# Optimization experiments

Hardware: AMD Instinct MI355X
Metric: run time of the kernel (lower is better)

The kernel has to match this reference:

```python
import jax, jax.numpy as jnp
import numpy as np

TEMP = 0.5
EPS = 1e-12


def setup_inputs() -> dict:
    key = jax.random.key(0)
    k1, k2, k3 = jax.random.split(key, 3)
    B, D = 2048, 512
    f_seq = jax.random.normal(k1, (B, 4, D), dtype=jnp.float32)
    f_spa = jax.random.normal(k2, (B, 4, D), dtype=jnp.float32)
    W = jax.random.normal(k3, (2 * D, D), dtype=jnp.float32) * 0.02
    b = jnp.zeros((D,), dtype=jnp.float32)
    return {"f_seq": f_seq, "f_spa": f_spa, "W": W, "b": b}


def _project_all(f, W, b):
    # pairs: (0,2), (1,2), (3,2) -> concat along batch dim => [3B, D]
    B = f.shape[0]
    left = jnp.transpose(f[:, jnp.array([0, 1, 3]), :], (1, 0, 2)).reshape(3 * B, -1)
    right = jnp.broadcast_to(f[:, 2, :][None], (3, B, f.shape[-1])).reshape(3 * B, -1)
    return jnp.concatenate([left, right], axis=-1) @ W + b


def reference(f_seq, f_spa, W, b):
    B = f_seq.shape[0]
    v_spa = _project_all(f_spa, W, b)  # [3B, D]
    v_seq = _project_all(f_seq, W, b)  # [3B, D]

    def normalize(x):
        n = jnp.sqrt(jnp.sum(x * x, axis=1, keepdims=True))
        return x / jnp.maximum(n, EPS)

    z = jnp.concatenate([normalize(v_spa), normalize(v_seq)], axis=0)  # [6B, D]
    sim = z @ z.T  # cosine sim of unit vectors, [6B, 6B]
    half = 3 * B
    idx = jnp.arange(half)
    pos = jnp.concatenate([sim[idx, idx + half], sim[idx + half, idx]])  # [6B]
    e = jnp.exp(sim / TEMP)
    denom = jnp.sum(e, axis=1) - jnp.diagonal(e)  # neg_mask zeros the diagonal
    loss = jnp.sum(-(pos / TEMP) + jnp.log(denom)) / (2.0 * half)
    return loss
```

## Files before the change

### kernel.cpp

```cpp
#include <hip/hip_runtime.h>
#include <hip/hip_bf16.h>
#include <cstdint>
#include <cstddef>

#define B_DIM 2048
#define D_DIM 512
#define NROWS 12288
#define HALF  6144
#define NTILE 96
#define NPAIR 4656
#define EXP_SCALE 2.8853900817779268f

typedef __attribute__((ext_vector_type(4))) float f32x4;
typedef __attribute__((ext_vector_type(8))) int i32x8;

__global__ __launch_bounds__(256) void gather_fp8(
    const float* __restrict__ f_seq, const float* __restrict__ f_spa,
    const float* __restrict__ W,
    unsigned char* __restrict__ A8, unsigned char* __restrict__ W8) {
  int gidx = blockIdx.x * 256 + threadIdx.x;
  if (blockIdx.x < 1536) {
    int r = gidx >> 5;
    int c = gidx & 31;
    int k0 = c << 5;
    const float* f = (r < HALF) ? f_spa : f_seq;
    int rr = (r < HALF) ? r : r - HALF;
    int p = rr >> 11;
    int i = rr & 2047;
    int sel = (p == 2) ? 3 : p;
    const float* src = (k0 < D_DIM) ? f + ((size_t)i * 4 + sel) * D_DIM + k0
                                    : f + ((size_t)i * 4 + 2) * D_DIM + (k0 - D_DIM);
    unsigned int d[8];
#pragma unroll
    for (int q = 0; q < 8; ++q) {
      float4 x = *(const float4*)(src + 4 * q);
      int pk = __builtin_amdgcn_cvt_pk_fp8_f32(x.x, x.y, 0, 0);
      pk     = __builtin_amdgcn_cvt_pk_fp8_f32(x.z, x.w, pk, 1);
      d[q] = (unsigned int)pk;
    }
    size_t off = (size_t)(r >> 7) * 131072 + (size_t)(c >> 2) * 16384 +
                 (size_t)(((r >> 4) & 7) * 2048 + (c & 3) * 512 + (r & 15) * 32);
    *(uint4*)(A8 + off)      = (uint4){d[0], d[1], d[2], d[3]};
    *(uint4*)(A8 + off + 16) = (uint4){d[4], d[5], d[6], d[7]};
  } else {
    int widx = gidx - 1536 * 256;
    int n = widx >> 5;
    int c = widx & 31;
    int k0 = c << 5;
    unsigned int d[8];
#pragma unroll
    for (int q = 0; q < 8; ++q) {
      float a0 = W[(size_t)(k0 + 4 * q + 0) * 512 + n] * 64.0f;
      float a1 = W[(size_t)(k0 + 4 * q + 1) * 512 + n] * 64.0f;
      float a2 = W[(size_t)(k0 + 4 * q + 2) * 512 + n] * 64.0f;
      float a3 = W[(size_t)(k0 + 4 * q + 3) * 512 + n] * 64.0f;
      int pk = __builtin_amdgcn_cvt_pk_fp8_f32(a0, a1, 0, 0);
      pk     = __builtin_amdgcn_cvt_pk_fp8_f32(a2, a3, pk, 1);
      d[q] = (unsigned int)pk;
    }
    size_t off = (size_t)(n >> 7) * 131072 + (size_t)(c >> 2) * 16384 +
                 (size_t)(((n >> 4) & 7) * 2048 + (c & 3) * 512 + (n & 15) * 32);
    *(uint4*)(W8 + off)      = (uint4){d[0], d[1], d[2], d[3]};
    *(uint4*)(W8 + off + 16) = (uint4){d[4], d[5], d[6], d[7]};
  }
}

__global__ __launch_bounds__(256, 4) void proj_fp8(
    const unsigned char* __restrict__ A8, const unsigned char* __restrict__ W8,
    const float* __restrict__ bvec, __hip_bfloat16* __restrict__ v) {
  int bn = blockIdx.x;
  int bm = blockIdx.y;
  int tid = threadIdx.x;
  int lane = tid & 63;
  int w = tid >> 6, wr = w >> 1, wc = w & 1;
  int g = lane >> 4, l16 = lane & 15;
  const unsigned char* pA = A8 + (size_t)bm * 131072 + (wr * 4) * 2048 + g * 512 + l16 * 32;
  const unsigned char* pB = W8 + (size_t)(bn >> 1) * 131072 +
                            ((bn & 1) * 4 + wc * 2) * 2048 + g * 512 + l16 * 32;
  f32x4 acc[4][2];
#pragma unroll
  for (int i = 0; i < 4; ++i)
#pragma unroll
    for (int j = 0; j < 2; ++j) acc[i][j] = (f32x4){0.f, 0.f, 0.f, 0.f};

#pragma unroll 1
  for (int t = 0; t < 8; ++t) {
    i32x8 bF[2];
#pragma unroll
    for (int ni = 0; ni < 2; ++ni)
      bF[ni] = *(const i32x8*)(pB + t * 16384 + ni * 2048);
#pragma unroll
    for (int mi = 0; mi < 4; ++mi) {
      i32x8 aF = *(const i32x8*)(pA + t * 16384 + mi * 2048);
#pragma unroll
      for (int ni = 0; ni < 2; ++ni)
        acc[mi][ni] = __builtin_amdgcn_mfma_scale_f32_16x16x128_f8f6f4(
            aF, bF[ni], acc[mi][ni], 0, 0,
            0, 0x7F7F7F7F, 0, 0x79797979);
    }
  }
  int grow0 = bm * 128 + wr * 64;
  int gcol0 = bn * 64 + wc * 32;
#pragma unroll
  for (int mi = 0; mi < 4; ++mi)
#pragma unroll
    for (int ni = 0; ni < 2; ++ni)
#pragma unroll
      for (int reg = 0; reg < 4; ++reg) {
        int grow = grow0 + mi * 16 + g * 4 + reg;
        int gcol = gcol0 + ni * 16 + l16;
        v[(size_t)grow * 512 + gcol] = __float2bfloat16(acc[mi][ni][reg] + bvec[gcol]);
      }
}

__global__ __launch_bounds__(256) void normalize_rows(
    const __hip_bfloat16* __restrict__ v, unsigned char* __restrict__ z) {
  int tid = threadIdx.x;
  int lane = tid & 63;
  int r = blockIdx.x * 4 + (tid >> 6);
  uint4 vv = *(const uint4*)(v + (size_t)r * 512 + lane * 8);
  float x[8];
  unsigned int uu[4] = {vv.x, vv.y, vv.z, vv.w};
#pragma unroll
  for (int q = 0; q < 4; ++q) {
    x[2 * q]     = __uint_as_float(uu[q] << 16);
    x[2 * q + 1] = __uint_as_float(uu[q] & 0xFFFF0000u);
  }
  float s = 0.f;
#pragma unroll
  for (int q = 0; q < 8; ++q) s += x[q] * x[q];
#pragma unroll
  for (int m = 1; m < 64; m <<= 1) s += __shfl_xor(s, m);
  float inv = 1.0f / fmaxf(sqrtf(s), 1e-12f);
  int pk0 = __builtin_amdgcn_cvt_pk_fp8_f32(x[0] * inv, x[1] * inv, 0, 0);
  pk0     = __builtin_amdgcn_cvt_pk_fp8_f32(x[2] * inv, x[3] * inv, pk0, 1);
  int pk1 = __builtin_amdgcn_cvt_pk_fp8_f32(x[4] * inv, x[5] * inv, 0, 0);
  pk1     = __builtin_amdgcn_cvt_pk_fp8_f32(x[6] * inv, x[7] * inv, pk1, 1);
  int k0 = lane * 8;
  size_t off = (size_t)(r >> 7) * 65536 + (size_t)(k0 >> 7) * 16384 +
               (size_t)(((r >> 4) & 7) * 2048 + ((k0 >> 5) & 3) * 512 +
                        (r & 15) * 32 + (k0 & 31));
  uint2 o = {(unsigned int)pk0, (unsigned int)pk1};
  *(uint2*)(z + off) = o;
}

__global__ __launch_bounds__(256, 4) void sim_fused_fp8(
    const unsigned char* __restrict__ z, float* __restrict__ partial,
    float* __restrict__ possim, float* __restrict__ selfsim) {
  __shared__ float wsum[2][128];
  __shared__ float csum[2][128];

  int l = blockIdx.x;
  int q = (l & 7) * 582 + (l >> 3);
  int si = 0, sj = 0, jj = q;
  for (;;) {
    int cnt = (si == sj) ? 78 : 144;
    if (jj < cnt) break;
    jj -= cnt;
    ++sj;
    if (sj == 8) { ++si; sj = si; }
  }
  int bi, bj;
  if (si == sj) {
    int rr = 0;
    while (jj >= 12 - rr) { jj -= 12 - rr; ++rr; }
    bi = si * 12 + rr; bj = si * 12 + rr + jj;
  } else {
    bi = si * 12 + jj / 12; bj = sj * 12 + jj % 12;
  }

  int tid = threadIdx.x;
  int lane = tid & 63;
  int w = tid >> 6, wr = w >> 1, wc = w & 1;
  int g = lane >> 4, l16 = lane & 15;

  const unsigned char* pA = z + (size_t)bi * 65536 + (size_t)(wr * 4) * 2048 + g * 512 + l16 * 32;
  const unsigned char* pB = z + (size_t)bj * 65536 + (size_t)(wc * 4) * 2048 + g * 512 + l16 * 32;

  f32x4 acc[4][4];
#pragma unroll
  for (int i = 0; i < 4; ++i)
#pragma unroll
    for (int j = 0; j < 4; ++j) acc[i][j] = (f32x4){0.f, 0.f, 0.f, 0.f};

#pragma unroll 1
  for (int t = 0; t < 4; ++t) {
    i32x8 bF[4];
#pragma unroll
    for (int ni = 0; ni < 4; ++ni)
      bF[ni] = *(const i32x8*)(pB + t * 16384 + ni * 2048);
#pragma unroll
    for (int mi = 0; mi < 4; ++mi) {
      i32x8 aF = *(const i32x8*)(pA + t * 16384 + mi * 2048);
#pragma unroll
      for (int ni = 0; ni < 4; ++ni)
        acc[mi][ni] = __builtin_amdgcn_mfma_scale_f32_16x16x128_f8f6f4(
            aF, bF[ni], acc[mi][ni], 0, 0,
            0, 0x7F7F7F7F, 0, 0x7F7F7F7F);
    }
  }

  bool diag = (bi == bj);
  bool posT = (bj == bi + 48);
  if ((diag || posT) && (wr == wc)) {
#pragma unroll
    for (int mi = 0; mi < 4; ++mi)
#pragma unroll
      for (int reg = 0; reg < 4; ++reg)
        if (l16 == g * 4 + reg) {
          int rl = wr * 64 + mi * 16 + g * 4 + reg;
          float sv = acc[mi][mi][reg];
          if (diag) selfsim[bi * 128 + rl] = sv;
          else      possim[bi * 128 + rl] = sv;
        }
  }
#pragma unroll
  for (int mi = 0; mi < 4; ++mi)
#pragma unroll
    for (int ni = 0; ni < 4; ++ni)
#pragma unroll
      for (int reg = 0; reg < 4; ++reg)
        acc[mi][ni][reg] = exp2f(acc[mi][ni][reg] * EXP_SCALE);
  float rs[4][4];
#pragma unroll
  for (int mi = 0; mi < 4; ++mi)
#pragma unroll
    for (int reg = 0; reg < 4; ++reg)
      rs[mi][reg] = acc[mi][0][reg] + acc[mi][1][reg] + acc[mi][2][reg] + acc[mi][3][reg];
#pragma unroll
  for (int m = 1; m < 16; m <<= 1)
#pragma unroll
    for (int mi = 0; mi < 4; ++mi)
#pragma unroll
      for (int reg = 0; reg < 4; ++reg)
        rs[mi][reg] += __shfl_xor(rs[mi][reg], m);
  if (l16 == 0) {
#pragma unroll
    for (int mi = 0; mi < 4; ++mi)
#pragma unroll
      for (int reg = 0; reg < 4; ++reg)
        wsum[wc][wr * 64 + mi * 16 + g * 4 + reg] = rs[mi][reg];
  }
  float cs[4];
#pragma unroll
  for (int ni = 0; ni < 4; ++ni) {
    float s = 0.f;
#pragma unroll
    for (int mi = 0; mi < 4; ++mi)
#pragma unroll
      for (int reg = 0; reg < 4; ++reg) s += acc[mi][ni][reg];
    s += __shfl_xor(s, 16);
    s += __shfl_xor(s, 32);
    cs[ni] = s;
  }
  if (g == 0) {
#pragma unroll
    for (int ni = 0; ni < 4; ++ni)
      csum[wr][wc * 64 + ni * 16 + l16] = cs[ni];
  }
  __syncthreads();
  if (tid < 128) {
    partial[(size_t)bj * NROWS + bi * 128 + tid] = wsum[0][tid] + wsum[1][tid];
    if (!diag)
      partial[(size_t)bi * NROWS + bj * 128 + tid] = csum[0][tid] + csum[1][tid];
  }
}

__global__ __launch_bounds__(256) void finalize_terms(
    const float* __restrict__ partial, const float* __restrict__ possim,
    const float* __restrict__ selfsim, float* __restrict__ blocksum) {
  int i = blockIdx.x * 256 + threadIdx.x;
  float s = 0.f;
  for (int bjt = 0; bjt < NTILE; ++bjt) s += partial[(size_t)bjt * NROWS + i];
  float denom = s - exp2f(selfsim[i] * EXP_SCALE);
  float pos = possim[(i < HALF) ? i : (i - HALF)];
  float term = -2.0f * pos + logf(denom);
#pragma unroll
  for (int m = 1; m < 64; m <<= 1) term += __shfl_xor(term, m);
  __shared__ float ws4[4];
  int tid = threadIdx.x, w = tid >> 6, lane = tid & 63;
  if (lane == 0) ws4[w] = term;
  __syncthreads();
  if (tid == 0) blocksum[blockIdx.x] = ws4[0] + ws4[1] + ws4[2] + ws4[3];
}

__global__ __launch_bounds__(64) void finalize_sum(
    const float* __restrict__ blocksum, float* __restrict__ out) {
  int tid = threadIdx.x;
  float s = (tid < 48) ? blocksum[tid] : 0.f;
#pragma unroll
  for (int m = 1; m < 64; m <<= 1) s += __shfl_xor(s, m);
  if (tid == 0) out[0] = s / 12288.0f;
}

extern "C" void kernel_launch(void* const* d_in, const int* in_sizes, int n_in,
                              void* d_out, int out_size, void* d_ws, size_t ws_size,
                              hipStream_t stream) {
  const float* f_seq = (const float*)d_in[0];
  const float* f_spa = (const float*)d_in[1];
  const float* W     = (const float*)d_in[2];
  const float* b     = (const float*)d_in[3];
  char* ws = (char*)d_ws;
  unsigned char* A8  = (unsigned char*)ws;
  unsigned char* W8  = (unsigned char*)(ws + 12582912);
  __hip_bfloat16* v  = (__hip_bfloat16*)(ws + 26214400);
  unsigned char* z   = (unsigned char*)ws;
  float* partial     = (float*)(ws + 12582912);
  float* possim      = (float*)(ws + 17301504);
  float* selfsim     = (float*)(ws + 17326080);
  float* blocksum    = (float*)(ws + 17375232);
  float* out         = (float*)d_out;

  gather_fp8<<<dim3(1600), dim3(256), 0, stream>>>(f_seq, f_spa, W, A8, W8);
  proj_fp8<<<dim3(8, 96), dim3(256), 0, stream>>>(A8, W8, b, v);
  normalize_rows<<<dim3(3072), dim3(256), 0, stream>>>(v, z);
  sim_fused_fp8<<<dim3(NPAIR), dim3(256), 0, stream>>>(z, partial, possim, selfsim);
  finalize_terms<<<dim3(48), dim3(256), 0, stream>>>(partial, possim, selfsim, blocksum);
  finalize_sum<<<dim3(1), dim3(64), 0, stream>>>(blocksum, out);
}
```

Baseline: 105.4 us.

## Shrink sim and projection tiles to single-wave 64x64 blocks

Both the projection and the symmetric similarity kernels now launch one 64-thread wave per block. Each wave computes a full 64x64 tile, so the shared-memory row and column reductions and __syncthreads are gone and partial sums are written straight from registers. The similarity grid grows to 18528 upper-triangular tile pairs over 192 tiles, and the finalize pass now sums 192 partials per row. Tiles are no longer shared between waves in a block, so each fragment load is reused less, and the larger partial buffer adds memory traffic; the workspace layout is moved to fit it.

```diff
diff --git a/kernel.cpp b/kernel.cpp
--- a/kernel.cpp
+++ b/kernel.cpp
@@ -7,8 +7,8 @@
 #define D_DIM 512
 #define NROWS 12288
 #define HALF  6144
-#define NTILE 96
-#define NPAIR 4656
+#define NT64  192
+#define NPAIR64 18528
 #define EXP_SCALE 2.8853900817779268f
 
 typedef __attribute__((ext_vector_type(4))) float f32x4;
@@ -65,46 +65,45 @@
   }
 }
 
-__global__ __launch_bounds__(256, 4) void proj_fp8(
+__global__ __launch_bounds__(64) void proj_fp8(
     const unsigned char* __restrict__ A8, const unsigned char* __restrict__ W8,
     const float* __restrict__ bvec, __hip_bfloat16* __restrict__ v) {
   int bn = blockIdx.x;
   int bm = blockIdx.y;
-  int tid = threadIdx.x;
-  int lane = tid & 63;
-  int w = tid >> 6, wr = w >> 1, wc = w & 1;
+  int lane = threadIdx.x & 63;
   int g = lane >> 4, l16 = lane & 15;
-  const unsigned char* pA = A8 + (size_t)bm * 131072 + (wr * 4) * 2048 + g * 512 + l16 * 32;
+  const unsigned char* pA = A8 + (size_t)(bm >> 1) * 131072 +
+                            ((bm & 1) * 4) * 2048 + g * 512 + l16 * 32;
   const unsigned char* pB = W8 + (size_t)(bn >> 1) * 131072 +
-                            ((bn & 1) * 4 + wc * 2) * 2048 + g * 512 + l16 * 32;
-  f32x4 acc[4][2];
+                            ((bn & 1) * 4) * 2048 + g * 512 + l16 * 32;
+  f32x4 acc[4][4];
 #pragma unroll
   for (int i = 0; i < 4; ++i)
 #pragma unroll
-    for (int j = 0; j < 2; ++j) acc[i][j] = (f32x4){0.f, 0.f, 0.f, 0.f};
+    for (int j = 0; j < 4; ++j) acc[i][j] = (f32x4){0.f, 0.f, 0.f, 0.f};
 
 #pragma unroll 1
   for (int t = 0; t < 8; ++t) {
-    i32x8 bF[2];
-#pragma unroll
-    for (int ni = 0; ni < 2; ++ni)
+    i32x8 bF[4];
+#pragma unroll
+    for (int ni = 0; ni < 4; ++ni)
       bF[ni] = *(const i32x8*)(pB + t * 16384 + ni * 2048);
 #pragma unroll
     for (int mi = 0; mi < 4; ++mi) {
       i32x8 aF = *(const i32x8*)(pA + t * 16384 + mi * 2048);
 #pragma unroll
-      for (int ni = 0; ni < 2; ++ni)
+      for (int ni = 0; ni < 4; ++ni)
         acc[mi][ni] = __builtin_amdgcn_mfma_scale_f32_16x16x128_f8f6f4(
             aF, bF[ni], acc[mi][ni], 0, 0,
             0, 0x7F7F7F7F, 0, 0x79797979);
     }
   }
-  int grow0 = bm * 128 + wr * 64;
-  int gcol0 = bn * 64 + wc * 32;
+  int grow0 = bm * 64;
+  int gcol0 = bn * 64;
 #pragma unroll
   for (int mi = 0; mi < 4; ++mi)
 #pragma unroll
-    for (int ni = 0; ni < 2; ++ni)
+    for (int ni = 0; ni < 4; ++ni)
 #pragma unroll
       for (int reg = 0; reg < 4; ++reg) {
         int grow = grow0 + mi * 16 + g * 4 + reg;
@@ -144,17 +143,14 @@
   *(uint2*)(z + off) = o;
 }
 
-__global__ __launch_bounds__(256, 4) void sim_fused_fp8(
+__global__ __launch_bounds__(64) void sim_fused_fp8(
     const unsigned char* __restrict__ z, float* __restrict__ partial,
     float* __restrict__ possim, float* __restrict__ selfsim) {
-  __shared__ float wsum[2][128];
-  __shared__ float csum[2][128];
-
   int l = blockIdx.x;
-  int q = (l & 7) * 582 + (l >> 3);
+  int q = (l & 7) * 2316 + (l >> 3);
   int si = 0, sj = 0, jj = q;
   for (;;) {
-    int cnt = (si == sj) ? 78 : 144;
+    int cnt = (si == sj) ? 300 : 576;
     if (jj < cnt) break;
     jj -= cnt;
     ++sj;
@@ -163,19 +159,19 @@
   int bi, bj;
   if (si == sj) {
     int rr = 0;
-    while (jj >= 12 - rr) { jj -= 12 - rr; ++rr; }
-    bi = si * 12 + rr; bj = si * 12 + rr + jj;
+    while (jj >= 24 - rr) { jj -= 24 - rr; ++rr; }
+    bi = si * 24 + rr; bj = si * 24 + rr + jj;
   } else {
-    bi = si * 12 + jj / 12; bj = sj * 12 + jj % 12;
-  }
-
-  int tid = threadIdx.x;
-  int lane = tid & 63;
-  int w = tid >> 6, wr = w >> 1, wc = w & 1;
+    bi = si * 24 + jj / 24; bj = sj * 24 + jj % 24;
+  }
+
+  int lane = threadIdx.x & 63;
   int g = lane >> 4, l16 = lane & 15;
 
-  const unsigned char* pA = z + (size_t)bi * 65536 + (size_t)(wr * 4) * 2048 + g * 512 + l16 * 32;
-  const unsigned char* pB = z + (size_t)bj * 65536 + (size_t)(wc * 4) * 2048 + g * 512 + l16 * 32;
+  const unsigned char* pA = z + (size_t)(bi >> 1) * 65536 +
+                            ((bi & 1) * 4) * 2048 + g * 512 + l16 * 32;
+  const unsigned char* pB = z + (size_t)(bj >> 1) * 65536 +
+                            ((bj & 1) * 4) * 2048 + g * 512 + l16 * 32;
 
   f32x4 acc[4][4];
 #pragma unroll
@@ -201,17 +197,17 @@
   }
 
   bool diag = (bi == bj);
-  bool posT = (bj == bi + 48);
-  if ((diag || posT) && (wr == wc)) {
+  bool posT = (bj == bi + 96);
+  if (diag || posT) {
 #pragma unroll
     for (int mi = 0; mi < 4; ++mi)
 #pragma unroll
       for (int reg = 0; reg < 4; ++reg)
         if (l16 == g * 4 + reg) {
-          int rl = wr * 64 + mi * 16 + g * 4 + reg;
+          int rl = mi * 16 + g * 4 + reg;
           float sv = acc[mi][mi][reg];
-          if (diag) selfsim[bi * 128 + rl] = sv;
-          else      possim[bi * 128 + rl] = sv;
+          if (diag) selfsim[bi * 64 + rl] = sv;
+          else      possim[bi * 64 + rl] = sv;
         }
   }
 #pragma unroll
@@ -239,30 +235,26 @@
     for (int mi = 0; mi < 4; ++mi)
 #pragma unroll
       for (int reg = 0; reg < 4; ++reg)
-        wsum[wc][wr * 64 + mi * 16 + g * 4 + reg] = rs[mi][reg];
-  }
-  float cs[4];
-#pragma unroll
-  for (int ni = 0; ni < 4; ++ni) {
-    float s = 0.f;
-#pragma unroll
-    for (int mi = 0; mi < 4; ++mi)
-#pragma unroll
-      for (int reg = 0; reg < 4; ++reg) s += acc[mi][ni][reg];
-    s += __shfl_xor(s, 16);
-    s += __shfl_xor(s, 32);
-    cs[ni] = s;
-  }
-  if (g == 0) {
-#pragma unroll
-    for (int ni = 0; ni < 4; ++ni)
-      csum[wr][wc * 64 + ni * 16 + l16] = cs[ni];
-  }
-  __syncthreads();
-  if (tid < 128) {
-    partial[(size_t)bj * NROWS + bi * 128 + tid] = wsum[0][tid] + wsum[1][tid];
-    if (!diag)
-      partial[(size_t)bi * NROWS + bj * 128 + tid] = csum[0][tid] + csum[1][tid];
+        partial[(size_t)bj * NROWS + bi * 64 + mi * 16 + g * 4 + reg] = rs[mi][reg];
+  }
+  if (!diag) {
+    float cs[4];
+#pragma unroll
+    for (int ni = 0; ni < 4; ++ni) {
+      float s = 0.f;
+#pragma unroll
+      for (int mi = 0; mi < 4; ++mi)
+#pragma unroll
+        for (int reg = 0; reg < 4; ++reg) s += acc[mi][ni][reg];
+      s += __shfl_xor(s, 16);
+      s += __shfl_xor(s, 32);
+      cs[ni] = s;
+    }
+    if (g == 0) {
+#pragma unroll
+      for (int ni = 0; ni < 4; ++ni)
+        partial[(size_t)bi * NROWS + bj * 64 + ni * 16 + l16] = cs[ni];
+    }
   }
 }
 
@@ -271,7 +263,7 @@
     const float* __restrict__ selfsim, float* __restrict__ blocksum) {
   int i = blockIdx.x * 256 + threadIdx.x;
   float s = 0.f;
-  for (int bjt = 0; bjt < NTILE; ++bjt) s += partial[(size_t)bjt * NROWS + i];
+  for (int bjt = 0; bjt < NT64; ++bjt) s += partial[(size_t)bjt * NROWS + i];
   float denom = s - exp2f(selfsim[i] * EXP_SCALE);
   float pos = possim[(i < HALF) ? i : (i - HALF)];
   float term = -2.0f * pos + logf(denom);
@@ -302,19 +294,19 @@
   const float* b     = (const float*)d_in[3];
   char* ws = (char*)d_ws;
   unsigned char* A8  = (unsigned char*)ws;
-  unsigned char* W8  = (unsigned char*)(ws + 12582912);
-  __hip_bfloat16* v  = (__hip_bfloat16*)(ws + 26214400);
   unsigned char* z   = (unsigned char*)ws;
   float* partial     = (float*)(ws + 12582912);
-  float* possim      = (float*)(ws + 17301504);
-  float* selfsim     = (float*)(ws + 17326080);
-  float* blocksum    = (float*)(ws + 17375232);
+  unsigned char* W8  = (unsigned char*)(ws + 22020096);
+  float* possim      = (float*)(ws + 22544384);
+  float* selfsim     = (float*)(ws + 22568960);
+  float* blocksum    = (float*)(ws + 22618112);
+  __hip_bfloat16* v  = (__hip_bfloat16*)(ws + 26214400);
   float* out         = (float*)d_out;
 
   gather_fp8<<<dim3(1600), dim3(256), 0, stream>>>(f_seq, f_spa, W, A8, W8);
-  proj_fp8<<<dim3(8, 96), dim3(256), 0, stream>>>(A8, W8, b, v);
+  proj_fp8<<<dim3(8, 192), dim3(64), 0, stream>>>(A8, W8, b, v);
   normalize_rows<<<dim3(3072), dim3(256), 0, stream>>>(v, z);
-  sim_fused_fp8<<<dim3(NPAIR), dim3(256), 0, stream>>>(z, partial, possim, selfsim);
+  sim_fused_fp8<<<dim3(NPAIR64), dim3(64), 0, stream>>>(z, partial, possim, selfsim);
   finalize_terms<<<dim3(48), dim3(256), 0, stream>>>(partial, possim, selfsim, blocksum);
   finalize_sum<<<dim3(1), dim3(64), 0, stream>>>(blocksum, out);
 }
```

Result: slower. 115.0 us (+9.1%).
